# Optimization experiments

Measured on AMD Instinct MI355X. Metric: run time of the kernel, lower is better.

Reference implementation:

```python
import jax, jax.numpy as jnp
import numpy as np

B, T, IN, OUT = 32, 2048, 1024, 256
DT = 1.0
TAU_MIN, TAU_MAX = 15.0, 25.0


def setup_inputs() -> dict:
    key = jax.random.key(0)
    k1, k2, k3 = jax.random.split(key, 3)
    inputs = jax.random.normal(k1, (B, T, IN), dtype=jnp.float32)
    bound = float(np.sqrt(1.0 / IN))
    weight = jax.random.uniform(k2, (OUT, IN), minval=-bound, maxval=bound, dtype=jnp.float32)
    bias = jnp.zeros((OUT,), dtype=jnp.float32)
    tau = jax.random.uniform(k3, (OUT,), minval=TAU_MIN, maxval=TAU_MAX, dtype=jnp.float32)
    decay = jnp.exp(-DT / tau)  # per-channel leak alpha in (0,1)
    return {"inputs": inputs, "weight": weight, "bias": bias, "decay": decay}


def reference(inputs, weight, bias, decay):
    # Dense projection: [B,T,IN] @ [IN,OUT] -> [B,T,OUT]
    current = jnp.einsum("bti,oi->bto", inputs, weight) + bias
    # Leaky integrator: u_t = alpha * u_{t-1} + (1-alpha) * x_t, u_0 = 0
    one_minus = 1.0 - decay

    def step(u, x):  # u,x: [B,OUT]
        u = decay * u + one_minus * x
        return u, u

    u0 = jnp.zeros((inputs.shape[0], weight.shape[0]), dtype=current.dtype)
    _, us = jax.lax.scan(step, u0, jnp.swapaxes(current, 0, 1))  # [T,B,OUT]
    return jnp.swapaxes(us, 0, 1)  # [B,T,OUT]
```

## Files before the change

### kernel.cpp

```cpp
#include <hip/hip_runtime.h>

#define B_   32
#define T_   2048
#define IN_  1024
#define OUT_ 256
#define M_   (B_ * T_)

#define BM 128
#define BN 256
#define BK 32
#define NSTEPS (IN_ / BK)
#define THREADS 512
#define TPB 16

#define LC 32
#define XPAD 264

#define ABUF_OFF(c) ((c) * (BM * BK * 2))
#define BBUF_OFF(c) (3 * (BM * BK * 2) + (c) * (BN * BK * 2))
#define XT_BYTES (BM * XPAD * 2)
#define SMEM_BYTES (XT_BYTES + 8192)

typedef __attribute__((ext_vector_type(4))) float f32x4;
typedef __attribute__((ext_vector_type(8))) __bf16 bf16x8;

__device__ __forceinline__ unsigned int f2bf_pk(float a, float b) {
    unsigned int ua = __float_as_uint(a);
    unsigned int ub = __float_as_uint(b);
    ua = (ua + 0x7fffu + ((ua >> 16) & 1u)) >> 16;
    ub = (ub + 0x7fffu + ((ub >> 16) & 1u)) >> 16;
    return ua | (ub << 16);
}
__device__ __forceinline__ unsigned short f2bf1(float a) {
    unsigned int ua = __float_as_uint(a);
    return (unsigned short)((ua + 0x7fffu + ((ua >> 16) & 1u)) >> 16);
}
__device__ __forceinline__ float bf2f(unsigned short s) {
    return __uint_as_float((unsigned int)s << 16);
}

__device__ __forceinline__ void gload_lds16(const void* g, void* l) {
    __builtin_amdgcn_global_load_lds(
        (const __attribute__((address_space(1))) void*)g,
        (__attribute__((address_space(3))) void*)l, 16, 0, 0);
}

__global__ __launch_bounds__(256) void convert_w_init(const float* __restrict__ W,
                                                      unsigned short* __restrict__ Wb,
                                                      unsigned int* __restrict__ flags) {
    const int i = blockIdx.x * 256 + threadIdx.x;
    const float4 v = ((const float4*)W)[i];
    uint2 o;
    o.x = f2bf_pk(v.x, v.y);
    o.y = f2bf_pk(v.z, v.w);
    ((uint2*)Wb)[i] = o;
    if (blockIdx.x == 0) {
        flags[threadIdx.x] = 0u;
        flags[256 + threadIdx.x] = 0u;
        if (threadIdx.x == 0) flags[512] = 0u;
    }
}

__global__ __launch_bounds__(THREADS, 4) void fused_all(
    const float* __restrict__ A, const unsigned short* __restrict__ Wb,
    const float* __restrict__ bias, const float* __restrict__ decay,
    float* __restrict__ out, float* __restrict__ localend,
    unsigned int* __restrict__ flags) {
    __shared__ __align__(16) char smem[SMEM_BYTES];
    __shared__ int s_tk;

    const int tid  = threadIdx.x;
    const int lane = tid & 63;
    const int wid  = tid >> 6;
    const int wm   = wid >> 2;
    const int wn   = wid & 3;
    const int l15  = lane & 15;
    const int l4   = lane >> 4;

    if (tid == 0) s_tk = (int)atomicAdd(&flags[512], 1u);
    __syncthreads();
    const int p    = s_tk;
    const int jb   = p & (TPB - 1);
    const int base = p - jb;
    const int bm0  = p * BM;

    const int rowA = tid >> 2;
    const int gA   = tid & 3;
    const float* gsrcA = A + (size_t)(bm0 + rowA) * IN_ + gA * 8;
    const int ldsA = rowA * BK + ((gA ^ (rowA & 3)) << 3);

    const unsigned short* gsrcB[2];
    int ldsBbase[2];
#pragma unroll
    for (int i = 0; i < 2; ++i) {
        const int q = (wid + i * 8) * 64 + lane;
        const int r = q >> 2;
        const int g = (q & 3) ^ (r & 3);
        gsrcB[i] = Wb + (size_t)r * IN_ + g * 8;
        ldsBbase[i] = (wid + i * 8) * 1024;
    }

    f32x4 acc[4][4] = {};
    float4 a0, a1;

    gload_lds16(gsrcB[0], smem + BBUF_OFF(0) + ldsBbase[0]);
    gload_lds16(gsrcB[1], smem + BBUF_OFF(0) + ldsBbase[1]);
    a0 = *(const float4*)(gsrcA);
    a1 = *(const float4*)(gsrcA + 4);
    {
        int4 w;
        w.x = f2bf_pk(a0.x, a0.y); w.y = f2bf_pk(a0.z, a0.w);
        w.z = f2bf_pk(a1.x, a1.y); w.w = f2bf_pk(a1.z, a1.w);
        *(int4*)(smem + ABUF_OFF(0) + ldsA * 2) = w;
    }
    a0 = *(const float4*)(gsrcA + BK);
    a1 = *(const float4*)(gsrcA + BK + 4);
    asm volatile("s_waitcnt lgkmcnt(0)" ::: "memory");
    __builtin_amdgcn_s_barrier();
    __builtin_amdgcn_sched_barrier(0);
    gload_lds16(gsrcB[0] + BK, smem + BBUF_OFF(1) + ldsBbase[0]);
    gload_lds16(gsrcB[1] + BK, smem + BBUF_OFF(1) + ldsBbase[1]);

    for (int i = 0; i < NSTEPS; ++i) {
        if (i + 1 < NSTEPS) {
            asm volatile("s_waitcnt vmcnt(2)" ::: "memory");
        } else {
            asm volatile("s_waitcnt vmcnt(0)" ::: "memory");
        }
        __builtin_amdgcn_sched_barrier(0);
        if (i + 1 < NSTEPS) {
            int4 w;
            w.x = f2bf_pk(a0.x, a0.y); w.y = f2bf_pk(a0.z, a0.w);
            w.z = f2bf_pk(a1.x, a1.y); w.w = f2bf_pk(a1.z, a1.w);
            *(int4*)(smem + ABUF_OFF((i + 1) % 3) + ldsA * 2) = w;
        }
        if (i + 2 < NSTEPS) {
            const int k0 = (i + 2) * BK;
            a0 = *(const float4*)(gsrcA + k0);
            a1 = *(const float4*)(gsrcA + k0 + 4);
        }
        asm volatile("s_waitcnt lgkmcnt(0)" ::: "memory");
        __builtin_amdgcn_s_barrier();
        __builtin_amdgcn_sched_barrier(0);
        if (i + 2 < NSTEPS) {
            const int k0 = (i + 2) * BK;
            gload_lds16(gsrcB[0] + k0, smem + BBUF_OFF((i + 2) % 3) + ldsBbase[0]);
            gload_lds16(gsrcB[1] + k0, smem + BBUF_OFF((i + 2) % 3) + ldsBbase[1]);
        }
        {
            const unsigned short* Ab = (const unsigned short*)(smem + ABUF_OFF(i % 3));
            const unsigned short* Bb = (const unsigned short*)(smem + BBUF_OFF(i % 3));
            bf16x8 af[4], bfv[4];
#pragma unroll
            for (int mi = 0; mi < 4; ++mi) {
                const int row = wm * 64 + mi * 16 + l15;
                af[mi] = *(const bf16x8*)&Ab[row * BK + ((l4 ^ (row & 3)) << 3)];
            }
#pragma unroll
            for (int ni = 0; ni < 4; ++ni) {
                const int col = wn * 64 + ni * 16 + l15;
                bfv[ni] = *(const bf16x8*)&Bb[col * BK + ((l4 ^ (col & 3)) << 3)];
            }
#pragma unroll
            for (int mi = 0; mi < 4; ++mi)
#pragma unroll
                for (int ni = 0; ni < 4; ++ni)
                    acc[mi][ni] = __builtin_amdgcn_mfma_f32_16x16x32_bf16(
                        af[mi], bfv[ni], acc[mi][ni], 0, 0, 0);
        }
    }
    __syncthreads();

    unsigned short* xt = (unsigned short*)smem;
    float* ceL = (float*)(smem + XT_BYTES);
    float* caL = ceL + 4 * OUT_;

#pragma unroll
    for (int ni = 0; ni < 4; ++ni) {
        const int col = wn * 64 + ni * 16 + l15;
        const float bv = bias[col];
#pragma unroll
        for (int mi = 0; mi < 4; ++mi) {
            const int r0 = wm * 64 + mi * 16 + (l4 << 2);
#pragma unroll
            for (int r = 0; r < 4; ++r)
                xt[(r0 + r) * XPAD + col] = f2bf1(acc[mi][ni][r] + bv);
        }
    }
    __syncthreads();

    for (int task = tid; task < 4 * OUT_; task += THREADS) {
        const int cl  = task >> 8;
        const int col = task & 255;
        const float alpha = decay[col];
        const float om = 1.0f - alpha;
        float u = 0.0f;
        const unsigned short* px = &xt[(cl * LC) * XPAD + col];
#pragma unroll
        for (int t = 0; t < LC; ++t)
            u = fmaf(alpha, u, om * bf2f(px[t * XPAD]));
        ceL[cl * OUT_ + col] = u;
    }
    __syncthreads();

    float a32 = 0.f, a128 = 0.f;
    if (tid < OUT_) {
        const float alpha_c = decay[tid];
        a32 = alpha_c;
#pragma unroll
        for (int i = 1; i < LC; ++i) a32 *= alpha_c;
        const float t2 = a32 * a32;
        a128 = t2 * t2;
        float le = ceL[tid];
        le = fmaf(a32, le, ceL[OUT_ + tid]);
        le = fmaf(a32, le, ceL[2 * OUT_ + tid]);
        le = fmaf(a32, le, ceL[3 * OUT_ + tid]);
        __hip_atomic_store(&localend[(size_t)p * OUT_ + tid], le,
                           __ATOMIC_RELAXED, __HIP_MEMORY_SCOPE_AGENT);
    }
    __syncthreads();
    if (tid == 0)
        __hip_atomic_store(&flags[p], 1u, __ATOMIC_RELEASE, __HIP_MEMORY_SCOPE_AGENT);
    if (tid < jb) {
        while (__hip_atomic_load(&flags[base + tid], __ATOMIC_ACQUIRE,
                                 __HIP_MEMORY_SCOPE_AGENT) == 0u)
            __builtin_amdgcn_s_sleep(2);
    }
    __syncthreads();

    if (tid < OUT_) {
        float cin = 0.0f;
#pragma unroll
        for (int i = 0; i < TPB - 1; ++i) {
            float v = __hip_atomic_load(&localend[(size_t)(base + i) * OUT_ + tid],
                                        __ATOMIC_RELAXED, __HIP_MEMORY_SCOPE_AGENT);
            if (i < jb) cin = fmaf(a128, cin, v);
        }
        caL[tid] = cin;
        const float c1 = fmaf(a32, cin, ceL[tid]);
        const float c2 = fmaf(a32, c1, ceL[OUT_ + tid]);
        const float c3 = fmaf(a32, c2, ceL[2 * OUT_ + tid]);
        caL[OUT_ + tid] = c1;
        caL[2 * OUT_ + tid] = c2;
        caL[3 * OUT_ + tid] = c3;
    }
    __syncthreads();

    for (int task = tid; task < 4 * OUT_; task += THREADS) {
        const int cl  = task >> 8;
        const int col = task & 255;
        const float alpha = decay[col];
        const float om = 1.0f - alpha;
        float u = caL[cl * OUT_ + col];
        const unsigned short* px = &xt[(cl * LC) * XPAD + col];
        float* po = &out[(size_t)(bm0 + cl * LC) * OUT_ + col];
#pragma unroll
        for (int t = 0; t < LC; ++t) {
            u = fmaf(alpha, u, om * bf2f(px[t * XPAD]));
            po[(size_t)t * OUT_] = u;
        }
    }
}

__global__ __launch_bounds__(256) void gemm_bias(const float* __restrict__ A,
                                                 const float* __restrict__ W,
                                                 const float* __restrict__ bias,
                                                 float* __restrict__ C) {
    __shared__ float As[16][64 + 4];
    __shared__ float Ws[16][64 + 4];
    const int bm = blockIdx.y * 64;
    const int bn = blockIdx.x * 64;
    const int tid = threadIdx.x;
    const int tx = tid & 15, ty = tid >> 4;
    const int lr = tid >> 2, lc = (tid & 3) << 2;
    float acc[4][4] = {};
    const float* Ap = A + (size_t)(bm + lr) * IN_ + lc;
    const float* Wp = W + (size_t)(bn + lr) * IN_ + lc;
    for (int k0 = 0; k0 < IN_; k0 += 16) {
        const float4 a = *(const float4*)(Ap + k0);
        const float4 w = *(const float4*)(Wp + k0);
        __syncthreads();
        As[lc + 0][lr] = a.x; As[lc + 1][lr] = a.y; As[lc + 2][lr] = a.z; As[lc + 3][lr] = a.w;
        Ws[lc + 0][lr] = w.x; Ws[lc + 1][lr] = w.y; Ws[lc + 2][lr] = w.z; Ws[lc + 3][lr] = w.w;
        __syncthreads();
#pragma unroll
        for (int kk = 0; kk < 16; ++kk) {
            const float4 av = *(const float4*)&As[kk][ty << 2];
            const float4 wv = *(const float4*)&Ws[kk][tx << 2];
            const float a0[4] = {av.x, av.y, av.z, av.w};
            const float w0[4] = {wv.x, wv.y, wv.z, wv.w};
#pragma unroll
            for (int i = 0; i < 4; ++i)
#pragma unroll
                for (int j = 0; j < 4; ++j) acc[i][j] = fmaf(a0[i], w0[j], acc[i][j]);
        }
    }
#pragma unroll
    for (int i = 0; i < 4; ++i) {
        const size_t row = (size_t)(bm + (ty << 2) + i);
#pragma unroll
        for (int j = 0; j < 4; ++j)
            C[row * OUT_ + bn + (tx << 2) + j] = acc[i][j] + bias[bn + (tx << 2) + j];
    }
}

__global__ __launch_bounds__(OUT_) void scan_simple(float* __restrict__ C,
                                                    const float* __restrict__ decay) {
    const int b = blockIdx.x;
    const int o = threadIdx.x;
    const float alpha = decay[o];
    const float om = 1.0f - alpha;
    float u = 0.0f;
    float* p = C + (size_t)b * T_ * OUT_ + o;
    for (int t = 0; t < T_; ++t) {
        const float x = p[(size_t)t * OUT_];
        u = fmaf(alpha, u, om * x);
        p[(size_t)t * OUT_] = u;
    }
}

extern "C" void kernel_launch(void* const* d_in, const int* in_sizes, int n_in,
                              void* d_out, int out_size, void* d_ws, size_t ws_size,
                              hipStream_t stream) {
    const float* inputs = (const float*)d_in[0];
    const float* weight = (const float*)d_in[1];
    const float* bias   = (const float*)d_in[2];
    const float* decay  = (const float*)d_in[3];
    float* out = (float*)d_out;

    const size_t wb_bytes = (size_t)OUT_ * IN_ * 2;
    const size_t le_bytes = (size_t)(M_ / BM) * OUT_ * 4;
    const size_t fl_bytes = 4096;
    const size_t need = wb_bytes + le_bytes + fl_bytes;

    if (ws_size >= need) {
        char* w = (char*)d_ws;
        unsigned short* Wb  = (unsigned short*)w;
        float* localend     = (float*)(w + wb_bytes);
        unsigned int* flags = (unsigned int*)(w + wb_bytes + le_bytes);

        convert_w_init<<<(OUT_ * IN_ / 4) / 256, 256, 0, stream>>>(weight, Wb, flags);
        fused_all<<<M_ / BM, THREADS, 0, stream>>>(inputs, Wb, bias, decay,
                                                   out, localend, flags);
    } else {
        dim3 g(OUT_ / 64, M_ / 64);
        gemm_bias<<<g, 256, 0, stream>>>(inputs, weight, bias, out);
        scan_simple<<<B_, OUT_, 0, stream>>>(out, decay);
    }
}
```

Before: 113.7 us.

## Stream fp32 A tiles directly to LDS via async loads, convert at fragment read

```diff
diff --git a/kernel.cpp b/kernel.cpp
--- a/kernel.cpp
+++ b/kernel.cpp
@@ -16,10 +16,10 @@
 #define LC 32
 #define XPAD 264
 
-#define ABUF_OFF(c) ((c) * (BM * BK * 2))
-#define BBUF_OFF(c) (3 * (BM * BK * 2) + (c) * (BN * BK * 2))
+#define ABUF_OFF(c) ((c) * 16384)
+#define BBUF_OFF(c) (49152 + (c) * 16384)
 #define XT_BYTES (BM * XPAD * 2)
-#define SMEM_BYTES (XT_BYTES + 8192)
+#define SMEM_BYTES 81920
 
 typedef __attribute__((ext_vector_type(4))) float f32x4;
 typedef __attribute__((ext_vector_type(8))) __bf16 bf16x8;
@@ -67,7 +67,6 @@
     float* __restrict__ out, float* __restrict__ localend,
     unsigned int* __restrict__ flags) {
     __shared__ __align__(16) char smem[SMEM_BYTES];
-    __shared__ int s_tk;
 
     const int tid  = threadIdx.x;
     const int lane = tid & 63;
@@ -77,84 +76,83 @@
     const int l15  = lane & 15;
     const int l4   = lane >> 4;
 
-    if (tid == 0) s_tk = (int)atomicAdd(&flags[512], 1u);
-    __syncthreads();
-    const int p    = s_tk;
+    if (tid == 0) *(int*)smem = (int)atomicAdd(&flags[512], 1u);
+    __syncthreads();
+    const int p = *(const int*)smem;
+    __syncthreads();
     const int jb   = p & (TPB - 1);
     const int base = p - jb;
     const int bm0  = p * BM;
 
-    const int rowA = tid >> 2;
-    const int gA   = tid & 3;
-    const float* gsrcA = A + (size_t)(bm0 + rowA) * IN_ + gA * 8;
-    const int ldsA = rowA * BK + ((gA ^ (rowA & 3)) << 3);
+    const float* gsrcA[2];
+    int ldsAbase[2];
+#pragma unroll
+    for (int j = 0; j < 2; ++j) {
+        const int q = (wid * 2 + j) * 64 + lane;
+        const int r = q >> 3;
+        const int g = (q & 7) ^ (r & 7);
+        gsrcA[j] = A + (size_t)(bm0 + r) * IN_ + g * 4;
+        ldsAbase[j] = (wid * 2 + j) * 1024;
+    }
 
     const unsigned short* gsrcB[2];
     int ldsBbase[2];
 #pragma unroll
-    for (int i = 0; i < 2; ++i) {
-        const int q = (wid + i * 8) * 64 + lane;
+    for (int j = 0; j < 2; ++j) {
+        const int q = (wid + j * 8) * 64 + lane;
         const int r = q >> 2;
         const int g = (q & 3) ^ (r & 3);
-        gsrcB[i] = Wb + (size_t)r * IN_ + g * 8;
-        ldsBbase[i] = (wid + i * 8) * 1024;
+        gsrcB[j] = Wb + (size_t)r * IN_ + g * 8;
+        ldsBbase[j] = (wid + j * 8) * 1024;
     }
 
     f32x4 acc[4][4] = {};
-    float4 a0, a1;
-
-    gload_lds16(gsrcB[0], smem + BBUF_OFF(0) + ldsBbase[0]);
-    gload_lds16(gsrcB[1], smem + BBUF_OFF(0) + ldsBbase[1]);
-    a0 = *(const float4*)(gsrcA);
-    a1 = *(const float4*)(gsrcA + 4);
-    {
-        int4 w;
-        w.x = f2bf_pk(a0.x, a0.y); w.y = f2bf_pk(a0.z, a0.w);
-        w.z = f2bf_pk(a1.x, a1.y); w.w = f2bf_pk(a1.z, a1.w);
-        *(int4*)(smem + ABUF_OFF(0) + ldsA * 2) = w;
-    }
-    a0 = *(const float4*)(gsrcA + BK);
-    a1 = *(const float4*)(gsrcA + BK + 4);
-    asm volatile("s_waitcnt lgkmcnt(0)" ::: "memory");
+
+#pragma unroll
+    for (int j = 0; j < 2; ++j) gload_lds16(gsrcB[j], smem + BBUF_OFF(0) + ldsBbase[j]);
+#pragma unroll
+    for (int j = 0; j < 2; ++j) gload_lds16(gsrcA[j], smem + ABUF_OFF(0) + ldsAbase[j]);
+#pragma unroll
+    for (int j = 0; j < 2; ++j) gload_lds16(gsrcA[j] + BK, smem + ABUF_OFF(1) + ldsAbase[j]);
+    asm volatile("s_waitcnt vmcnt(0)" ::: "memory");
+    __builtin_amdgcn_sched_barrier(0);
     __builtin_amdgcn_s_barrier();
     __builtin_amdgcn_sched_barrier(0);
-    gload_lds16(gsrcB[0] + BK, smem + BBUF_OFF(1) + ldsBbase[0]);
-    gload_lds16(gsrcB[1] + BK, smem + BBUF_OFF(1) + ldsBbase[1]);
 
     for (int i = 0; i < NSTEPS; ++i) {
-        if (i + 1 < NSTEPS) {
+        if (i == NSTEPS - 1) {
+            asm volatile("s_waitcnt vmcnt(0)" ::: "memory");
+        } else {
             asm volatile("s_waitcnt vmcnt(2)" ::: "memory");
-        } else {
-            asm volatile("s_waitcnt vmcnt(0)" ::: "memory");
-        }
+        }
+        __builtin_amdgcn_sched_barrier(0);
+        __builtin_amdgcn_s_barrier();
         __builtin_amdgcn_sched_barrier(0);
         if (i + 1 < NSTEPS) {
-            int4 w;
-            w.x = f2bf_pk(a0.x, a0.y); w.y = f2bf_pk(a0.z, a0.w);
-            w.z = f2bf_pk(a1.x, a1.y); w.w = f2bf_pk(a1.z, a1.w);
-            *(int4*)(smem + ABUF_OFF((i + 1) % 3) + ldsA * 2) = w;
+            const int k0 = (i + 1) * BK;
+#pragma unroll
+            for (int j = 0; j < 2; ++j)
+                gload_lds16(gsrcB[j] + k0, smem + BBUF_OFF((i + 1) & 1) + ldsBbase[j]);
         }
         if (i + 2 < NSTEPS) {
             const int k0 = (i + 2) * BK;
-            a0 = *(const float4*)(gsrcA + k0);
-            a1 = *(const float4*)(gsrcA + k0 + 4);
-        }
-        asm volatile("s_waitcnt lgkmcnt(0)" ::: "memory");
-        __builtin_amdgcn_s_barrier();
-        __builtin_amdgcn_sched_barrier(0);
-        if (i + 2 < NSTEPS) {
-            const int k0 = (i + 2) * BK;
-            gload_lds16(gsrcB[0] + k0, smem + BBUF_OFF((i + 2) % 3) + ldsBbase[0]);
-            gload_lds16(gsrcB[1] + k0, smem + BBUF_OFF((i + 2) % 3) + ldsBbase[1]);
+#pragma unroll
+            for (int j = 0; j < 2; ++j)
+                gload_lds16(gsrcA[j] + k0, smem + ABUF_OFF((i + 2) % 3) + ldsAbase[j]);
         }
         {
-            const unsigned short* Ab = (const unsigned short*)(smem + ABUF_OFF(i % 3));
-            const unsigned short* Bb = (const unsigned short*)(smem + BBUF_OFF(i % 3));
+            const float* Ab = (const float*)(smem + ABUF_OFF(i % 3));
+            const unsigned short* Bb = (const unsigned short*)(smem + BBUF_OFF(i & 1));
             bf16x8 af[4], bfv[4];
 #pragma unroll
             for (int mi = 0; mi < 4; ++mi) {
                 const int row = wm * 64 + mi * 16 + l15;
-                af[mi] = *(const bf16x8*)&Ab[row * BK + ((l4 ^ (row & 3)) << 3)];
+                const float4 x0 = *(const float4*)&Ab[row * 32 + (((2 * l4)     ^ (row & 7)) << 2)];
+                const float4 x1 = *(const float4*)&Ab[row * 32 + (((2 * l4 + 1) ^ (row & 7)) << 2)];
+                union { uint4 u; bf16x8 v; } t;
+                t.u.x = f2bf_pk(x0.x, x0.y); t.u.y = f2bf_pk(x0.z, x0.w);
+                t.u.z = f2bf_pk(x1.x, x1.y); t.u.w = f2bf_pk(x1.z, x1.w);
+                af[mi] = t.v;
             }
 #pragma unroll
             for (int ni = 0; ni < 4; ++ni) {
```

After: 118.2 us. +4.0%, slower.
